# Performance work log

Measured on AMD Instinct MI355X. Metric: run time of the kernel, lower is better.

The kernel has to match this reference:

```python
import jax, jax.numpy as jnp
import numpy as np
from jax import lax


def setup_inputs() -> dict:
    key = jax.random.key(0)
    ks = jax.random.split(key, 8)
    b, l, d_model = 2, 1024, 768
    expand, d_state, d_conv = 2, 16, 4
    d_inner = d_model * expand            # 1536
    dt_rank = -(-d_model // 16)           # ceil(768/16) = 48
    x = jax.random.normal(ks[0], (b, l, d_model), jnp.float32)
    W_in = jax.random.normal(ks[1], (d_model, 2 * d_inner), jnp.float32) * 0.02
    conv_w = jax.random.normal(ks[2], (d_inner, 1, d_conv), jnp.float32) * 0.1
    conv_b = jnp.zeros((d_inner,), jnp.float32)
    W_x = jax.random.normal(ks[3], (d_inner, dt_rank + 2 * d_state), jnp.float32) * 0.02
    W_dt = jax.random.normal(ks[4], (dt_rank, d_inner), jnp.float32) * 0.02
    b_dt = jax.random.normal(ks[5], (d_inner,), jnp.float32) * 0.02
    # A_log = log(1..d_state) broadcast over d_inner, as in the module init
    A_log = jnp.broadcast_to(jnp.log(jnp.arange(1, d_state + 1, dtype=jnp.float32)), (d_inner, d_state)).copy()
    D = jnp.ones((d_inner,), jnp.float32)
    W_out = jax.random.normal(ks[6], (d_inner, d_model), jnp.float32) * 0.02
    return {"x": x, "W_in": W_in, "conv_w": conv_w, "conv_b": conv_b, "W_x": W_x,
            "W_dt": W_dt, "b_dt": b_dt, "A_log": A_log, "D": D, "W_out": W_out}


def _silu(v):
    return v * jax.nn.sigmoid(v)


def reference(x, W_in, conv_w, conv_b, W_x, W_dt, b_dt, A_log, D, W_out):
    b, l, d_model = x.shape
    d_inner, _, d_conv = conv_w.shape
    dt_rank = W_dt.shape[0]
    n = A_log.shape[1]

    # in_proj and split into x / res paths
    x_and_res = x @ W_in                              # (b, l, 2*d_inner)
    xi, res = jnp.split(x_and_res, 2, axis=-1)

    # depthwise causal conv1d (torch pads d_conv-1 both sides then slices [:l])
    xc = jnp.transpose(xi, (0, 2, 1))                 # (b, d_inner, l)
    xc = lax.conv_general_dilated(
        xc, conv_w, window_strides=(1,), padding=[(d_conv - 1, 0)],
        dimension_numbers=("NCH", "OIH", "NCH"), feature_group_count=d_inner)
    xc = xc + conv_b[None, :, None]
    u = _silu(jnp.transpose(xc, (0, 2, 1)))           # (b, l, d_inner)

    # SSM parameters (input-dependent)
    A = -jnp.exp(A_log.astype(jnp.float32))           # (d_inner, n)
    x_dbl = u @ W_x                                   # (b, l, dt_rank + 2n)
    delta = x_dbl[..., :dt_rank]
    B = x_dbl[..., dt_rank:dt_rank + n]               # (b, l, n)
    C = x_dbl[..., dt_rank + n:]                      # (b, l, n)
    delta = jax.nn.softplus(delta @ W_dt + b_dt)      # (b, l, d_inner)

    # discretize
    deltaA = jnp.exp(delta[..., None] * A)            # (b, l, d_inner, n)
    deltaB_u = delta[..., None] * B[:, :, None, :] * u[..., None]  # (b, l, d_inner, n)

    # parallel associative scan over l: h_t = deltaA_t * h_{t-1} + deltaB_u_t
    def combine(c1, c2):
        a1, b1 = c1
        a2, b2 = c2
        return (a1 * a2, a2 * b1 + b2)

    _, hs = lax.associative_scan(combine, (deltaA, deltaB_u), axis=1)  # (b, l, d_inner, n)

    y = jnp.einsum("bldn,bln->bld", hs, C) + u * D    # (b, l, d_inner)
    y = y * _silu(res)
    out = y @ W_out                                   # (b, l, d_model)
    return out
```

## Files before the change

### kernel.cpp

```cpp
#include <hip/hip_runtime.h>
#include <math.h>

#define DI 1536
#define DM 768
#define NSTATE 16
#define DTRANK 48
#define LSEQ 1024
#define NBATCH 2
#define MROWS (NBATCH*LSEQ)
#define NXR 3072
#define NCHUNK 128
#define CLEN 8
#define SCB 128
#define DMP 16

typedef __attribute__((ext_vector_type(4))) float f32x4;
typedef __attribute__((ext_vector_type(8))) short s16x8;
typedef __attribute__((ext_vector_type(4))) unsigned int u32x4;

__device__ __forceinline__ unsigned short f2bf(float f) {
  unsigned int x = __builtin_bit_cast(unsigned int, f);
  return (unsigned short)((x + 0x7fffu + ((x >> 16) & 1u)) >> 16);
}

__device__ __forceinline__ void gload_lds16(const void* g, void* l) {
  __builtin_amdgcn_global_load_lds(
      (const __attribute__((address_space(1))) void*)g,
      (__attribute__((address_space(3))) void*)l, 16, 0, 0);
}

__global__ __launch_bounds__(256) void prep_kernel(
    const float* __restrict__ x, const float* __restrict__ W_in,
    const float* __restrict__ W_out, const float* __restrict__ W_x,
    unsigned short* __restrict__ x_bf, unsigned short* __restrict__ WinT,
    unsigned short* __restrict__ WoutT, unsigned short* __restrict__ WxT)
{
  __shared__ float t[32][33];
  const int bid = blockIdx.x;
  const int tid = threadIdx.x;
  if (bid < 768) {
    long i = ((long)bid * 256 + tid) * 8;
    f32x4 v0 = *(const f32x4*)&x[i];
    f32x4 v1 = *(const f32x4*)&x[i + 4];
    unsigned short o[8];
    #pragma unroll
    for (int j = 0; j < 4; ++j) { o[j] = f2bf(v0[j]); o[4 + j] = f2bf(v1[j]); }
    *(u32x4*)&x_bf[i] = *(u32x4*)o;
    return;
  }
  const float* in; unsigned short* out; int R, C, bx, by; bool guard = false;
  if (bid < 3072)      { int q = bid - 768;  in = W_in;  out = WinT;  R = DM; C = NXR; bx = q % 96; by = q / 96; }
  else if (bid < 4224) { int q = bid - 3072; in = W_out; out = WoutT; R = DI; C = DM;  bx = q % 24; by = q / 24; }
  else                 { int q = bid - 4224; in = W_x;   out = WxT;   R = DI; C = 80;  bx = q % 3;  by = q / 3; guard = true; }
  int ctile = bx * 32, rtile = by * 32;
  int tx = tid & 31, ty = tid >> 5;
  #pragma unroll
  for (int i = 0; i < 4; ++i) {
    int r = ty + i * 8;
    if (!guard || (rtile + r < R && ctile + tx < C))
      t[r][tx] = in[(long)(rtile + r) * C + ctile + tx];
  }
  __syncthreads();
  #pragma unroll
  for (int i = 0; i < 4; ++i) {
    int cc = ty + i * 8;
    if (!guard || (ctile + cc < C && rtile + tx < R))
      out[(long)(ctile + cc) * R + rtile + tx] = f2bf(t[tx][cc]);
  }
}

template<int FM, int FN>
__global__ __launch_bounds__(256) void gemm_bf16(
    const unsigned short* __restrict__ A,
    const unsigned short* __restrict__ BT,
    float* __restrict__ C, int M, int N, int K)
{
  constexpr int BM = 32 * FM, BN = 32 * FN;
  constexpr int TM = BM / 16, TN = BN / 16;
  __shared__ unsigned short Ap[BM * 32];
  __shared__ unsigned short Bp[BN * 32];
  const int tid = threadIdx.x;
  const int lane = tid & 63, wave = tid >> 6;
  const int wr = wave >> 1, wc = wave & 1;
  const int lg = lane >> 4, lr = lane & 15;
  const int m0 = blockIdx.y * BM, n0 = blockIdx.x * BN;
  f32x4 acc[FM][FN] = {};
  for (int k0 = 0; k0 < K; k0 += 32) {
    #pragma unroll
    for (int p = 0; p < TM / 4; ++p) {
      int tile = wave + p * 4;
      gload_lds16(&A[(long)(m0 + tile * 16 + lr) * K + k0 + lg * 8], &Ap[tile * 512]);
    }
    #pragma unroll
    for (int p = 0; p < TN / 4; ++p) {
      int tile = wave + p * 4;
      gload_lds16(&BT[(long)(n0 + tile * 16 + lr) * K + k0 + lg * 8], &Bp[tile * 512]);
    }
    __syncthreads();
    s16x8 af[FM], bfr[FN];
    #pragma unroll
    for (int m = 0; m < FM; ++m)
      af[m] = *(s16x8*)&Ap[(((wr * FM + m) * 4 + lg) * 16 + lr) * 8];
    #pragma unroll
    for (int n = 0; n < FN; ++n)
      bfr[n] = *(s16x8*)&Bp[(((wc * FN + n) * 4 + lg) * 16 + lr) * 8];
    #pragma unroll
    for (int m = 0; m < FM; ++m)
      #pragma unroll
      for (int n = 0; n < FN; ++n)
        acc[m][n] = __builtin_amdgcn_mfma_f32_16x16x32_bf16(af[m], bfr[n], acc[m][n], 0, 0, 0);
    __syncthreads();
  }
  #pragma unroll
  for (int m = 0; m < FM; ++m)
    #pragma unroll
    for (int n = 0; n < FN; ++n)
      #pragma unroll
      for (int r = 0; r < 4; ++r) {
        int row = m0 + wr * 16 * FM + m * 16 + lg * 4 + r;
        int col = n0 + wc * 16 * FN + n * 16 + lr;
        C[(long)row * N + col] = acc[m][n][r];
      }
}

__global__ __launch_bounds__(256) void conv_silu_kernel(
    const float* __restrict__ xr,
    const float* __restrict__ conv_w,
    const float* __restrict__ conv_b,
    float* __restrict__ u,
    unsigned short* __restrict__ u_bf)
{
  int idx = blockIdx.x * 256 + threadIdx.x;
  if (idx >= MROWS * DI) return;
  int c = idx % DI;
  int bm = idx / DI;
  int t = bm % LSEQ;
  int b = bm / LSEQ;
  float w0 = conv_w[c * 4 + 0], w1 = conv_w[c * 4 + 1];
  float w2 = conv_w[c * 4 + 2], w3 = conv_w[c * 4 + 3];
  const float* xc = xr + (long)b * LSEQ * NXR + c;
  float acc = conv_b[c];
  if (t >= 3) acc = fmaf(xc[(long)(t - 3) * NXR], w0, acc);
  if (t >= 2) acc = fmaf(xc[(long)(t - 2) * NXR], w1, acc);
  if (t >= 1) acc = fmaf(xc[(long)(t - 1) * NXR], w2, acc);
  acc = fmaf(xc[(long)t * NXR], w3, acc);
  float s = acc / (1.f + __expf(-acc));
  u[idx] = s;
  u_bf[idx] = f2bf(s);
}

__global__ __launch_bounds__(256) void xdbl_mfma(
    const unsigned short* __restrict__ u_bf,
    const unsigned short* __restrict__ WxT,
    float* __restrict__ xdbl)
{
  const int tid = threadIdx.x;
  const int lane = tid & 63, wave = tid >> 6;
  const int lg = lane >> 4, lr = lane & 15;
  const int m0 = blockIdx.x * 16;
  f32x4 acc[5] = {};
  const int kbase = wave * (DI / 4);
  #pragma unroll
  for (int kk = 0; kk < DI / 4; kk += 32) {
    int k0 = kbase + kk;
    s16x8 af = *(const s16x8*)&u_bf[(long)(m0 + lr) * DI + k0 + lg * 8];
    #pragma unroll
    for (int n = 0; n < 5; ++n) {
      s16x8 bfr = *(const s16x8*)&WxT[(long)(n * 16 + lr) * DI + k0 + lg * 8];
      acc[n] = __builtin_amdgcn_mfma_f32_16x16x32_bf16(af, bfr, acc[n], 0, 0, 0);
    }
  }
  __shared__ float red[4][16][80];
  #pragma unroll
  for (int n = 0; n < 5; ++n)
    #pragma unroll
    for (int r = 0; r < 4; ++r)
      red[wave][lg * 4 + r][n * 16 + lr] = acc[n][r];
  __syncthreads();
  for (int i = tid; i < 16 * 80; i += 256) {
    int row = i / 80, col = i % 80;
    float s = red[0][row][col] + red[1][row][col] + red[2][row][col] + red[3][row][col];
    xdbl[(long)(m0 + row) * 80 + col] = s;
  }
}

__global__ __launch_bounds__(256) void delta_kernel(
    const float* __restrict__ xdbl,
    const float* __restrict__ W_dt,
    const float* __restrict__ b_dt,
    float* __restrict__ delta)
{
  __shared__ float sx[DMP][DTRANK];
  const int tid = threadIdx.x;
  const int c = blockIdx.x * 256 + tid;
  const int m0 = blockIdx.y * DMP;
  for (int i = tid; i < DMP * DTRANK; i += 256) {
    int mm = i / DTRANK, r = i % DTRANK;
    sx[mm][r] = xdbl[(long)(m0 + mm) * 80 + r];
  }
  __syncthreads();
  float bias = b_dt[c];
  float acc[DMP];
  #pragma unroll
  for (int mm = 0; mm < DMP; ++mm) acc[mm] = bias;
  for (int r = 0; r < DTRANK; ++r) {
    float wv = W_dt[(long)r * DI + c];
    #pragma unroll
    for (int mm = 0; mm < DMP; ++mm)
      acc[mm] = fmaf(sx[mm][r], wv, acc[mm]);
  }
  #pragma unroll
  for (int mm = 0; mm < DMP; ++mm) {
    float v = acc[mm];
    float sp = (v > 20.f) ? v : log1pf(__expf(v));
    delta[(long)(m0 + mm) * DI + c] = sp;
  }
}

__global__ __launch_bounds__(SCB) void scan_ph1(
    const float* __restrict__ delta,
    const float* __restrict__ xdbl,
    const float* __restrict__ u,
    const float* __restrict__ A_log,
    float* __restrict__ Aprod,
    float* __restrict__ Hend)
{
  const int b = blockIdx.z, chunk = blockIdx.y;
  const int tid = threadIdx.x;
  const int d = blockIdx.x * SCB + tid;
  const long mbase = (long)b * LSEQ + chunk * CLEN;
  __shared__ float sB[CLEN][NSTATE];
  for (int i = tid; i < CLEN * NSTATE; i += SCB) {
    int t = i >> 4, j = i & 15;
    sB[t][j] = xdbl[(mbase + t) * 80 + DTRANK + j];
  }
  __syncthreads();
  float a[NSTATE];
  #pragma unroll
  for (int n = 0; n < NSTATE; ++n)
    a[n] = -__expf(A_log[(long)d * NSTATE + n]);
  float h[NSTATE] = {};
  float Ap[NSTATE];
  #pragma unroll
  for (int n = 0; n < NSTATE; ++n) Ap[n] = 1.f;
  #pragma unroll
  for (int t = 0; t < CLEN; ++t) {
    long m = mbase + t;
    float dt = delta[m * DI + d];
    float uu = u[m * DI + d];
    float dtu = dt * uu;
    #pragma unroll
    for (int n = 0; n < NSTATE; ++n) {
      float dA = __expf(dt * a[n]);
      Ap[n] *= dA;
      h[n] = fmaf(dA, h[n], dtu * sB[t][n]);
    }
  }
  long o = (((long)b * NCHUNK + chunk) * DI + d) * NSTATE;
  #pragma unroll
  for (int q = 0; q < 4; ++q) {
    f32x4 va = { Ap[q*4+0], Ap[q*4+1], Ap[q*4+2], Ap[q*4+3] };
    f32x4 vh = { h[q*4+0], h[q*4+1], h[q*4+2], h[q*4+3] };
    *(f32x4*)&Aprod[o + q*4] = va;
    *(f32x4*)&Hend[o + q*4] = vh;
  }
}

__global__ __launch_bounds__(256) void scan_ph2(
    const float* __restrict__ Aprod,
    const float* __restrict__ Hend,
    float* __restrict__ Hstart)
{
  int idx = blockIdx.x * 256 + threadIdx.x;
  int b = idx / (DI * NSTATE);
  int r = idx % (DI * NSTATE);
  long o = (long)b * NCHUNK * DI * NSTATE + r;
  const long stride = (long)DI * NSTATE;
  float h = 0.f;
  for (int c = 0; c < NCHUNK; ++c) {
    float Ap = Aprod[o + c * stride];
    float He = Hend[o + c * stride];
    Hstart[o + c * stride] = h;
    h = fmaf(Ap, h, He);
  }
}

__global__ __launch_bounds__(SCB) void scan_ph3(
    const float* __restrict__ delta,
    const float* __restrict__ xdbl,
    const float* __restrict__ u,
    const float* __restrict__ xr,
    const float* __restrict__ A_log,
    const float* __restrict__ Dp,
    const float* __restrict__ Hstart,
    unsigned short* __restrict__ yg)
{
  const int b = blockIdx.z, chunk = blockIdx.y;
  const int tid = threadIdx.x;
  const int d = blockIdx.x * SCB + tid;
  const long mbase = (long)b * LSEQ + chunk * CLEN;
  __shared__ float sB[CLEN][NSTATE], sC[CLEN][NSTATE];
  for (int i = tid; i < CLEN * NSTATE; i += SCB) {
    int t = i >> 4, j = i & 15;
    long mo = (mbase + t) * 80 + DTRANK + j;
    sB[t][j] = xdbl[mo];
    sC[t][j] = xdbl[mo + NSTATE];
  }
  __syncthreads();
  float a[NSTATE];
  #pragma unroll
  for (int n = 0; n < NSTATE; ++n)
    a[n] = -__expf(A_log[(long)d * NSTATE + n]);
  const float Dv = Dp[d];
  long o = (((long)b * NCHUNK + chunk) * DI + d) * NSTATE;
  float h[NSTATE];
  #pragma unroll
  for (int q = 0; q < 4; ++q) {
    f32x4 vh = *(const f32x4*)&Hstart[o + q*4];
    h[q*4+0] = vh[0]; h[q*4+1] = vh[1]; h[q*4+2] = vh[2]; h[q*4+3] = vh[3];
  }
  #pragma unroll
  for (int t = 0; t < CLEN; ++t) {
    long m = mbase + t;
    float dt = delta[m * DI + d];
    float uu = u[m * DI + d];
    float rr = xr[m * NXR + DI + d];
    float dtu = dt * uu;
    float p0 = 0.f, p1 = 0.f, p2 = 0.f, p3 = 0.f;
    #pragma unroll
    for (int q = 0; q < 4; ++q) {
      float dA0 = __expf(dt * a[q*4+0]);
      float dA1 = __expf(dt * a[q*4+1]);
      float dA2 = __expf(dt * a[q*4+2]);
      float dA3 = __expf(dt * a[q*4+3]);
      h[q*4+0] = fmaf(dA0, h[q*4+0], dtu * sB[t][q*4+0]);
      h[q*4+1] = fmaf(dA1, h[q*4+1], dtu * sB[t][q*4+1]);
      h[q*4+2] = fmaf(dA2, h[q*4+2], dtu * sB[t][q*4+2]);
      h[q*4+3] = fmaf(dA3, h[q*4+3], dtu * sB[t][q*4+3]);
    }
    #pragma unroll
    for (int n = 0; n < NSTATE; n += 4) {
      p0 = fmaf(h[n+0], sC[t][n+0], p0);
      p1 = fmaf(h[n+1], sC[t][n+1], p1);
      p2 = fmaf(h[n+2], sC[t][n+2], p2);
      p3 = fmaf(h[n+3], sC[t][n+3], p3);
    }
    float yv = (p0 + p1) + (p2 + p3) + uu * Dv;
    float gate = rr / (1.f + __expf(-rr));
    yg[m * DI + d] = f2bf(yv * gate);
  }
}

extern "C" void kernel_launch(void* const* d_in, const int* in_sizes, int n_in,
                              void* d_out, int out_size, void* d_ws, size_t ws_size,
                              hipStream_t stream)
{
  const float* x      = (const float*)d_in[0];
  const float* W_in   = (const float*)d_in[1];
  const float* conv_w = (const float*)d_in[2];
  const float* conv_b = (const float*)d_in[3];
  const float* W_x    = (const float*)d_in[4];
  const float* W_dt   = (const float*)d_in[5];
  const float* b_dt   = (const float*)d_in[6];
  const float* A_log  = (const float*)d_in[7];
  const float* Dp     = (const float*)d_in[8];
  const float* W_out  = (const float*)d_in[9];
  float* out = (float*)d_out;

  char* p = (char*)d_ws;
  float* xr     = (float*)(p + 0);
  float* u      = (float*)(p + 25165824);
  unsigned short* u_bf = (unsigned short*)(p + 37748736);
  float* xdbl   = (float*)(p + 44040192);
  float* delta  = (float*)(p + 44695552);
  float* Aprod  = (float*)(p + 57278464);
  float* Hend   = (float*)(p + 82444288);
  float* Hstart = (float*)(p + 107610112);
  unsigned short* yg    = (unsigned short*)(p + 132775936);
  unsigned short* x_bf  = (unsigned short*)(p + 139067392);
  unsigned short* WinT  = (unsigned short*)(p + 142213120);
  unsigned short* WoutT = (unsigned short*)(p + 146931712);
  unsigned short* WxT   = (unsigned short*)(p + 149291008);

  prep_kernel<<<4368, 256, 0, stream>>>(x, W_in, W_out, W_x, x_bf, WinT, WoutT, WxT);
  gemm_bf16<4, 4><<<dim3(NXR / 128, MROWS / 128), 256, 0, stream>>>(
      x_bf, WinT, xr, MROWS, NXR, DM);
  conv_silu_kernel<<<(MROWS * DI + 255) / 256, 256, 0, stream>>>(xr, conv_w, conv_b, u, u_bf);
  xdbl_mfma<<<MROWS / 16, 256, 0, stream>>>(u_bf, WxT, xdbl);
  delta_kernel<<<dim3(DI / 256, MROWS / DMP), 256, 0, stream>>>(xdbl, W_dt, b_dt, delta);
  scan_ph1<<<dim3(DI / SCB, NCHUNK, NBATCH), SCB, 0, stream>>>(
      delta, xdbl, u, A_log, Aprod, Hend);
  scan_ph2<<<(NBATCH * DI * NSTATE) / 256, 256, 0, stream>>>(Aprod, Hend, Hstart);
  scan_ph3<<<dim3(DI / SCB, NCHUNK, NBATCH), SCB, 0, stream>>>(
      delta, xdbl, u, xr, A_log, Dp, Hstart, yg);
  gemm_bf16<2, 2><<<dim3(DM / 64, MROWS / 64), 256, 0, stream>>>(
      yg, WoutT, out, MROWS, DM, DI);
}
```

Measured before the change: 166.9 us.

## Transpose scan state layout to state-major, precompute -exp(A_log), reuse Hend in place

```diff
diff --git a/kernel.cpp b/kernel.cpp
--- a/kernel.cpp
+++ b/kernel.cpp
@@ -32,8 +32,10 @@
 __global__ __launch_bounds__(256) void prep_kernel(
     const float* __restrict__ x, const float* __restrict__ W_in,
     const float* __restrict__ W_out, const float* __restrict__ W_x,
+    const float* __restrict__ A_log,
     unsigned short* __restrict__ x_bf, unsigned short* __restrict__ WinT,
-    unsigned short* __restrict__ WoutT, unsigned short* __restrict__ WxT)
+    unsigned short* __restrict__ WoutT, unsigned short* __restrict__ WxT,
+    float* __restrict__ negA)
 {
   __shared__ float t[32][33];
   const int bid = blockIdx.x;
@@ -48,12 +50,27 @@
     *(u32x4*)&x_bf[i] = *(u32x4*)o;
     return;
   }
+  int tx = tid & 31, ty = tid >> 5;
+  if (bid >= 4368) {
+    int rtile = (bid - 4368) * 32;
+    #pragma unroll
+    for (int i = 0; i < 4; ++i) {
+      int r = ty + i * 8;
+      if (tx < 16) t[r][tx] = A_log[(long)(rtile + r) * NSTATE + tx];
+    }
+    __syncthreads();
+    #pragma unroll
+    for (int i = 0; i < 2; ++i) {
+      int cc = ty + i * 8;
+      negA[(long)cc * DI + rtile + tx] = -__expf(t[tx][cc]);
+    }
+    return;
+  }
   const float* in; unsigned short* out; int R, C, bx, by; bool guard = false;
   if (bid < 3072)      { int q = bid - 768;  in = W_in;  out = WinT;  R = DM; C = NXR; bx = q % 96; by = q / 96; }
   else if (bid < 4224) { int q = bid - 3072; in = W_out; out = WoutT; R = DI; C = DM;  bx = q % 24; by = q / 24; }
   else                 { int q = bid - 4224; in = W_x;   out = WxT;   R = DI; C = 80;  bx = q % 3;  by = q / 3; guard = true; }
   int ctile = bx * 32, rtile = by * 32;
-  int tx = tid & 31, ty = tid >> 5;
   #pragma unroll
   for (int i = 0; i < 4; ++i) {
     int r = ty + i * 8;
@@ -221,7 +238,7 @@
     const float* __restrict__ delta,
     const float* __restrict__ xdbl,
     const float* __restrict__ u,
-    const float* __restrict__ A_log,
+    const float* __restrict__ negA,
     float* __restrict__ Aprod,
     float* __restrict__ Hend)
 {
@@ -238,7 +255,7 @@
   float a[NSTATE];
   #pragma unroll
   for (int n = 0; n < NSTATE; ++n)
-    a[n] = -__expf(A_log[(long)d * NSTATE + n]);
+    a[n] = negA[(long)n * DI + d];
   float h[NSTATE] = {};
   float Ap[NSTATE];
   #pragma unroll
@@ -256,20 +273,17 @@
       h[n] = fmaf(dA, h[n], dtu * sB[t][n]);
     }
   }
-  long o = (((long)b * NCHUNK + chunk) * DI + d) * NSTATE;
-  #pragma unroll
-  for (int q = 0; q < 4; ++q) {
-    f32x4 va = { Ap[q*4+0], Ap[q*4+1], Ap[q*4+2], Ap[q*4+3] };
-    f32x4 vh = { h[q*4+0], h[q*4+1], h[q*4+2], h[q*4+3] };
-    *(f32x4*)&Aprod[o + q*4] = va;
-    *(f32x4*)&Hend[o + q*4] = vh;
+  const long o = ((long)(b * NCHUNK + chunk) * NSTATE) * DI + d;
+  #pragma unroll
+  for (int n = 0; n < NSTATE; ++n) {
+    Aprod[o + (long)n * DI] = Ap[n];
+    Hend[o + (long)n * DI] = h[n];
   }
 }
 
 __global__ __launch_bounds__(256) void scan_ph2(
     const float* __restrict__ Aprod,
-    const float* __restrict__ Hend,
-    float* __restrict__ Hstart)
+    float* __restrict__ Hend)
 {
   int idx = blockIdx.x * 256 + threadIdx.x;
   int b = idx / (DI * NSTATE);
@@ -280,7 +294,7 @@
   for (int c = 0; c < NCHUNK; ++c) {
     float Ap = Aprod[o + c * stride];
     float He = Hend[o + c * stride];
-    Hstart[o + c * stride] = h;
+    Hend[o + c * stride] = h;
     h = fmaf(Ap, h, He);
   }
 }
@@ -290,7 +304,7 @@
     const float* __restrict__ xdbl,
     const float* __restrict__ u,
     const float* __restrict__ xr,
-    const float* __restrict__ A_log,
+    const float* __restrict__ negA,
     const float* __restrict__ Dp,
     const float* __restrict__ Hstart,
     unsigned short* __restrict__ yg)
@@ -310,15 +324,13 @@
   float a[NSTATE];
   #pragma unroll
   for (int n = 0; n < NSTATE; ++n)
-    a[n] = -__expf(A_log[(long)d * NSTATE + n]);
+    a[n] = negA[(long)n * DI + d];
   const float Dv = Dp[d];
-  long o = (((long)b * NCHUNK + chunk) * DI + d) * NSTATE;
+  const long o = ((long)(b * NCHUNK + chunk) * NSTATE) * DI + d;
   float h[NSTATE];
   #pragma unroll
-  for (int q = 0; q < 4; ++q) {
-    f32x4 vh = *(const f32x4*)&Hstart[o + q*4];
-    h[q*4+0] = vh[0]; h[q*4+1] = vh[1]; h[q*4+2] = vh[2]; h[q*4+3] = vh[3];
-  }
+  for (int n = 0; n < NSTATE; ++n)
+    h[n] = Hstart[o + (long)n * DI];
   #pragma unroll
   for (int t = 0; t < CLEN; ++t) {
     long m = mbase + t;
@@ -375,24 +387,25 @@
   float* delta  = (float*)(p + 44695552);
   float* Aprod  = (float*)(p + 57278464);
   float* Hend   = (float*)(p + 82444288);
-  float* Hstart = (float*)(p + 107610112);
-  unsigned short* yg    = (unsigned short*)(p + 132775936);
-  unsigned short* x_bf  = (unsigned short*)(p + 139067392);
-  unsigned short* WinT  = (unsigned short*)(p + 142213120);
-  unsigned short* WoutT = (unsigned short*)(p + 146931712);
-  unsigned short* WxT   = (unsigned short*)(p + 149291008);
-
-  prep_kernel<<<4368, 256, 0, stream>>>(x, W_in, W_out, W_x, x_bf, WinT, WoutT, WxT);
+  unsigned short* yg    = (unsigned short*)(p + 107610112);
+  unsigned short* x_bf  = (unsigned short*)(p + 113901568);
+  unsigned short* WinT  = (unsigned short*)(p + 117047296);
+  unsigned short* WoutT = (unsigned short*)(p + 121765888);
+  unsigned short* WxT   = (unsigned short*)(p + 124125184);
+  float* negA   = (float*)(p + 124370944);
+
+  prep_kernel<<<4416, 256, 0, stream>>>(x, W_in, W_out, W_x, A_log,
+                                        x_bf, WinT, WoutT, WxT, negA);
   gemm_bf16<4, 4><<<dim3(NXR / 128, MROWS / 128), 256, 0, stream>>>(
       x_bf, WinT, xr, MROWS, NXR, DM);
   conv_silu_kernel<<<(MROWS * DI + 255) / 256, 256, 0, stream>>>(xr, conv_w, conv_b, u, u_bf);
   xdbl_mfma<<<MROWS / 16, 256, 0, stream>>>(u_bf, WxT, xdbl);
   delta_kernel<<<dim3(DI / 256, MROWS / DMP), 256, 0, stream>>>(xdbl, W_dt, b_dt, delta);
   scan_ph1<<<dim3(DI / SCB, NCHUNK, NBATCH), SCB, 0, stream>>>(
-      delta, xdbl, u, A_log, Aprod, Hend);
-  scan_ph2<<<(NBATCH * DI * NSTATE) / 256, 256, 0, stream>>>(Aprod, Hend, Hstart);
+      delta, xdbl, u, negA, Aprod, Hend);
+  scan_ph2<<<(NBATCH * DI * NSTATE) / 256, 256, 0, stream>>>(Aprod, Hend);
   scan_ph3<<<dim3(DI / SCB, NCHUNK, NBATCH), SCB, 0, stream>>>(
-      delta, xdbl, u, xr, A_log, Dp, Hstart, yg);
+      delta, xdbl, u, xr, negA, Dp, Hend, yg);
   gemm_bf16<2, 2><<<dim3(DM / 64, MROWS / 64), 256, 0, stream>>>(
       yg, WoutT, out, MROWS, DM, DI);
 }
```

New measurement: 160.1 us. 4.1% less time.
